# Optimization experiments

Hardware: AMD Instinct MI355X
Metric: run time of the kernel (lower is better)

## Reference

```python
import jax, jax.numpy as jnp
import numpy as np

N_NODES, N_EDGES, N_RELS, D_IN, D_OUT = 50000, 200000, 64, 32, 32


def setup_inputs() -> dict:
    key = jax.random.key(0)
    k1, k2, k3, k4, k5 = jax.random.split(key, 5)
    feat = jax.random.normal(k1, (N_NODES, D_IN), dtype=jnp.float32)
    # learned per-relation projection weights: [R, D_IN, D_OUT]
    weight = jax.random.normal(k2, (N_RELS, D_IN, D_OUT), dtype=jnp.float32) * 0.05
    src = jax.random.randint(k3, (N_EDGES,), 0, N_NODES)
    dst = jax.random.randint(k4, (N_EDGES,), 0, N_NODES)
    etypes = jax.random.randint(k5, (N_EDGES,), 0, N_RELS)
    return {"feat": feat, "weight": weight, "src": src, "dst": dst, "etypes": etypes}


def reference(feat, weight, src, dst, etypes):
    # gather source features and per-edge relation weights (HighMem variant
    # materializes W[etypes] just like torch index_select), then per-edge bmm
    n_nodes = feat.shape[0]
    msg = jnp.einsum('ei,eio->eo', feat[src], weight[etypes])  # [E, D_OUT]
    out = jax.ops.segment_sum(msg, dst, num_segments=n_nodes)  # [N, D_OUT]
    return out
```

## Files before the change

kernel.cpp:

```cpp
#include <hip/hip_runtime.h>


#define D 32
#define NRELS 64
#define BLOCK 1024
#define WPB (BLOCK / 64)
#define GRID 256
#define MAXCHUNK 1024
#define MAXTILES (NRELS + MAXCHUNK / 16)

typedef __bf16 bf16x8 __attribute__((ext_vector_type(8)));
typedef float  f32x4  __attribute__((ext_vector_type(4)));

static __device__ __forceinline__ unsigned int f2b(float x) {
    unsigned int u = __float_as_uint(x);
    return (u + 0x7fffu + ((u >> 16) & 1u)) >> 16;
}


__global__ __launch_bounds__(256) void prep_kernel(
    const float* __restrict__ feat, const float* __restrict__ weight,
    unsigned short* __restrict__ featb,
    unsigned short* __restrict__ wpack,
    int n_nodes)
{
    int idx = blockIdx.x * 256 + threadIdx.x;
    int nfeat = n_nodes * 4;
    if (idx < nfeat) {
        const float4* fp = (const float4*)(feat + (size_t)idx * 8);
        float4 a = fp[0], b = fp[1];
        uint4 o;
        o.x = f2b(a.x) | (f2b(a.y) << 16);
        o.y = f2b(a.z) | (f2b(a.w) << 16);
        o.z = f2b(b.x) | (f2b(b.y) << 16);
        o.w = f2b(b.z) | (f2b(b.w) << 16);
        ((uint4*)featb)[idx] = o;
    } else if (idx < nfeat + NRELS * 2 * 64) {
        int t = idx - nfeat;
        int r = t >> 7, half = (t >> 6) & 1, lane = t & 63;
        int quad = lane >> 4, n = lane & 15;
        const float* W = weight + (size_t)r * (D * D) + half * 16 + n;
        uint4 o;
        unsigned int v[8];
        #pragma unroll
        for (int j = 0; j < 8; ++j) v[j] = f2b(W[(quad * 8 + j) * D]);
        o.x = v[0] | (v[1] << 16);
        o.y = v[2] | (v[3] << 16);
        o.z = v[4] | (v[5] << 16);
        o.w = v[6] | (v[7] << 16);
        ((uint4*)wpack)[t] = o;
    }
}


__global__ __launch_bounds__(BLOCK, 4) void rgcn_fused_kernel(
    const unsigned short* __restrict__ featb,
    const unsigned short* __restrict__ wpack,
    const int* __restrict__ src,
    const int* __restrict__ dst,
    const int* __restrict__ etypes,
    float* __restrict__ out,
    int E, int chunk)
{
    __shared__ int cnt[NRELS];
    __shared__ int off[NRELS];
    __shared__ unsigned short list[MAXCHUNK];
    __shared__ unsigned short desc[MAXTILES];
    __shared__ int ntile_sh;

    int tid = threadIdx.x;
    int gbase = blockIdx.x * chunk;

    if (tid < NRELS) cnt[tid] = 0;
    __syncthreads();

    int my_r = -1, my_rank = 0;
    if (tid < chunk && gbase + tid < E) {
        my_r = etypes[gbase + tid];
        my_rank = atomicAdd(&cnt[my_r], 1);
    }
    __syncthreads();

    if (tid < 64) {
        int c = cnt[tid];
        int x = c;
        #pragma unroll
        for (int o = 1; o < 64; o <<= 1) {
            int y = __shfl_up(x, o, 64);
            if (tid >= o) x += y;
        }
        off[tid] = x - c;

        int nt = (c + 15) >> 4;
        int tx = nt;
        #pragma unroll
        for (int o = 1; o < 64; o <<= 1) {
            int y = __shfl_up(tx, o, 64);
            if (tid >= o) tx += y;
        }
        int tbase = tx - nt;
        for (int t = 0; t < nt; ++t)
            desc[tbase + t] = (unsigned short)((tid << 8) | t);
        if (tid == 63) ntile_sh = tx;
    }
    __syncthreads();

    if (my_r >= 0) list[off[my_r] + my_rank] = (unsigned short)tid;
    int ntiles = ntile_sh;
    __syncthreads();

    int wave = tid >> 6;
    int lane = tid & 63;
    int n    = lane & 15;
    int quad = lane >> 4;

    int per = (ntiles + WPB - 1) / WPB;
    int t0 = wave * per;
    int t1 = t0 + per; if (t1 > ntiles) t1 = ntiles;

    for (int ti = t0; ti < t1; ++ti) {
        int dsc = desc[ti];
        int r = dsc >> 8;
        int t = dsc & 255;
        int c = cnt[r];
        int mbase = t * 16;
        int mcnt = c - mbase; if (mcnt > 16) mcnt = 16;
        int lbase = off[r] + mbase;

        bf16x8 b0 = *(const bf16x8*)(wpack + ((size_t)(r * 2 + 0) * 64 + lane) * 8);
        bf16x8 b1 = *(const bf16x8*)(wpack + ((size_t)(r * 2 + 1) * 64 + lane) * 8);

        int mm = (n < mcnt) ? n : 0;
        int le = list[lbase + mm];
        int s  = src[gbase + le];
        bf16x8 a = *(const bf16x8*)(featb + (size_t)s * D + quad * 8);

        f32x4 z = {0.f, 0.f, 0.f, 0.f};
        f32x4 c0 = __builtin_amdgcn_mfma_f32_16x16x32_bf16(a, b0, z, 0, 0, 0);
        f32x4 c1 = __builtin_amdgcn_mfma_f32_16x16x32_bf16(a, b1, z, 0, 0, 0);

        #pragma unroll
        for (int v = 0; v < 4; ++v) {
            int m2 = quad * 4 + v;
            if (m2 < mcnt) {
                int le2 = list[lbase + m2];
                int d = dst[gbase + le2];
                atomicAdd(out + (size_t)d * D + n,      c0[v]);
                atomicAdd(out + (size_t)d * D + 16 + n, c1[v]);
            }
        }
    }
}


__global__ __launch_bounds__(256) void rgcn_edge_kernel(
    const float* __restrict__ feat, const float* __restrict__ weight,
    const int* __restrict__ src, const int* __restrict__ dst,
    const int* __restrict__ etypes, float* __restrict__ out, int n_edges)
{
    int gid = blockIdx.x * blockDim.x + threadIdx.x;
    int e = gid >> 5;
    int o = gid & 31;
    if (e >= n_edges) return;
    int s = src[e], d = dst[e], r = etypes[e];
    const float* W = weight + (size_t)r * (D * D);
    float fv = feat[(size_t)s * D + o];
    float acc = 0.f;
    #pragma unroll
    for (int i = 0; i < D; ++i) {
        float fi = __shfl(fv, i, 32);
        acc = fmaf(fi, W[i * D + o], acc);
    }
    atomicAdd(&out[(size_t)d * D + o], acc);
}


extern "C" void kernel_launch(void* const* d_in, const int* in_sizes, int n_in,
                              void* d_out, int out_size, void* d_ws, size_t ws_size,
                              hipStream_t stream) {
    const float* feat   = (const float*)d_in[0];
    const float* weight = (const float*)d_in[1];
    const int*   src    = (const int*)d_in[2];
    const int*   dst    = (const int*)d_in[3];
    const int*   etypes = (const int*)d_in[4];
    float*       out    = (float*)d_out;

    int N = in_sizes[0] / D;
    int R = in_sizes[1] / (D * D);
    int E = in_sizes[2];

    hipMemsetAsync(d_out, 0, (size_t)out_size * sizeof(float), stream);

    int chunk = (E + GRID - 1) / GRID;
    size_t featb_elems = (size_t)N * D;
    size_t need = (featb_elems + (size_t)NRELS * 2 * 64 * 8) * sizeof(unsigned short);

    if (R != NRELS || chunk > MAXCHUNK || ws_size < need) {
        long long total = (long long)E * 32;
        int grid = (int)((total + 255) / 256);
        rgcn_edge_kernel<<<grid, 256, 0, stream>>>(feat, weight, src, dst,
                                                   etypes, out, E);
        return;
    }

    unsigned short* featb = (unsigned short*)d_ws;
    unsigned short* wpack = featb + featb_elems;

    int prep_tasks = N * 4 + NRELS * 2 * 64;
    int prep_grid = (prep_tasks + 255) / 256;
    prep_kernel<<<prep_grid, 256, 0, stream>>>(feat, weight, featb, wpack, N);

    rgcn_fused_kernel<<<GRID, BLOCK, 0, stream>>>(featb, wpack, src, dst,
                                                  etypes, out, E, chunk);
}
```

Before: 94.25 us.

## Replace float atomic scatter with CSR-by-destination bucketing and segmented gather

Builds a per-destination histogram and a two-kernel prefix scan to get CSR offsets. Each edge gets a slot in a message buffer sorted by destination. The MFMA kernel now writes messages to those slots with plain stores instead of atomics to the output. A final gather kernel sums each node's contiguous messages. This removes the contention and cost of float atomics on the output, but adds several launches, an integer histogram with atomics, a slot-assignment atomic, and an E x 32 float staging buffer written and then read back.

```diff
diff --git a/kernel.cpp b/kernel.cpp
--- a/kernel.cpp
+++ b/kernel.cpp
@@ -20,12 +20,15 @@
 
 __global__ __launch_bounds__(256) void prep_kernel(
     const float* __restrict__ feat, const float* __restrict__ weight,
+    const int* __restrict__ dst,
     unsigned short* __restrict__ featb,
     unsigned short* __restrict__ wpack,
-    int n_nodes)
+    int* __restrict__ hist,
+    int n_nodes, int E)
 {
     int idx = blockIdx.x * 256 + threadIdx.x;
     int nfeat = n_nodes * 4;
+    int nw = NRELS * 2 * 64;
     if (idx < nfeat) {
         const float4* fp = (const float4*)(feat + (size_t)idx * 8);
         float4 a = fp[0], b = fp[1];
@@ -35,7 +38,7 @@
         o.z = f2b(b.x) | (f2b(b.y) << 16);
         o.w = f2b(b.z) | (f2b(b.w) << 16);
         ((uint4*)featb)[idx] = o;
-    } else if (idx < nfeat + NRELS * 2 * 64) {
+    } else if (idx < nfeat + nw) {
         int t = idx - nfeat;
         int r = t >> 7, half = (t >> 6) & 1, lane = t & 63;
         int quad = lane >> 4, n = lane & 15;
@@ -49,23 +52,88 @@
         o.z = v[4] | (v[5] << 16);
         o.w = v[6] | (v[7] << 16);
         ((uint4*)wpack)[t] = o;
-    }
-}
-
-
-__global__ __launch_bounds__(BLOCK, 4) void rgcn_fused_kernel(
+    } else if (idx < nfeat + nw + E) {
+        int e = idx - nfeat - nw;
+        atomicAdd(&hist[dst[e]], 1);
+    }
+}
+
+
+__global__ __launch_bounds__(256) void scan1_kernel(
+    const int* __restrict__ hist, int* __restrict__ off,
+    int* __restrict__ bsum, int N)
+{
+    __shared__ int wsum[4];
+    int t = threadIdx.x;
+    int idx = blockIdx.x * 1024 + t * 4;
+    int4 v = {0, 0, 0, 0};
+    if (idx + 3 < N) v = *(const int4*)(hist + idx);
+    else {
+        if (idx     < N) v.x = hist[idx];
+        if (idx + 1 < N) v.y = hist[idx + 1];
+        if (idx + 2 < N) v.z = hist[idx + 2];
+        if (idx + 3 < N) v.w = hist[idx + 3];
+    }
+    int s0 = v.x, s1 = s0 + v.y, s2 = s1 + v.z, s3 = s2 + v.w;
+    int x = s3;
+    #pragma unroll
+    for (int o = 1; o < 64; o <<= 1) {
+        int y = __shfl_up(x, o, 64);
+        if ((t & 63) >= o) x += y;
+    }
+    if ((t & 63) == 63) wsum[t >> 6] = x;
+    __syncthreads();
+    int w = t >> 6;
+    int wbase = 0;
+    #pragma unroll
+    for (int i = 0; i < 4; ++i) if (i < w) wbase += wsum[i];
+    int excl = wbase + x - s3;
+    if (idx     < N) off[idx]     = excl;
+    if (idx + 1 < N) off[idx + 1] = excl + s0;
+    if (idx + 2 < N) off[idx + 2] = excl + s1;
+    if (idx + 3 < N) off[idx + 3] = excl + s2;
+    if (t == 255) bsum[blockIdx.x] = wbase + x;
+}
+
+
+__global__ __launch_bounds__(256) void scan2_kernel(
+    int* __restrict__ off, const int* __restrict__ bsum,
+    int N, int E, int nblk)
+{
+    __shared__ int sbase;
+    int t = threadIdx.x;
+    if (t < 64) {
+        int v = (t < (int)blockIdx.x && t < nblk) ? bsum[t] : 0;
+        #pragma unroll
+        for (int o = 32; o > 0; o >>= 1) v += __shfl_down(v, o, 64);
+        if (t == 0) sbase = v;
+    }
+    __syncthreads();
+    int base = sbase;
+    int idx = blockIdx.x * 1024 + t * 4;
+    #pragma unroll
+    for (int k = 0; k < 4; ++k)
+        if (idx + k < N) off[idx + k] += base;
+    if (blockIdx.x == 0 && t == 0) off[N] = E;
+}
+
+
+__global__ __launch_bounds__(BLOCK, 4) void rgcn_compute_kernel(
     const unsigned short* __restrict__ featb,
     const unsigned short* __restrict__ wpack,
     const int* __restrict__ src,
     const int* __restrict__ dst,
     const int* __restrict__ etypes,
-    float* __restrict__ out,
+    const int* __restrict__ off,
+    int* __restrict__ cur,
+    float* __restrict__ msg,
     int E, int chunk)
 {
     __shared__ int cnt[NRELS];
-    __shared__ int off[NRELS];
+    __shared__ int offr[NRELS];
     __shared__ unsigned short list[MAXCHUNK];
     __shared__ unsigned short desc[MAXTILES];
+    __shared__ int slot_sh[MAXCHUNK];
     __shared__ int ntile_sh;
 
     int tid = threadIdx.x;
@@ -76,8 +144,11 @@
 
     int my_r = -1, my_rank = 0;
     if (tid < chunk && gbase + tid < E) {
-        my_r = etypes[gbase + tid];
+        int e = gbase + tid;
+        my_r = etypes[e];
         my_rank = atomicAdd(&cnt[my_r], 1);
+        int d = dst[e];
+        slot_sh[tid] = off[d] + atomicAdd(&cur[d], 1);
     }
     __syncthreads();
 
@@ -89,7 +160,7 @@
             int y = __shfl_up(x, o, 64);
             if (tid >= o) x += y;
         }
-        off[tid] = x - c;
+        offr[tid] = x - c;
 
         int nt = (c + 15) >> 4;
         int tx = nt;
@@ -105,7 +176,7 @@
     }
     __syncthreads();
 
-    if (my_r >= 0) list[off[my_r] + my_rank] = (unsigned short)tid;
+    if (my_r >= 0) list[offr[my_r] + my_rank] = (unsigned short)tid;
     int ntiles = ntile_sh;
     __syncthreads();
 
@@ -125,7 +196,7 @@
         int c = cnt[r];
         int mbase = t * 16;
         int mcnt = c - mbase; if (mcnt > 16) mcnt = 16;
-        int lbase = off[r] + mbase;
+        int lbase = offr[r] + mbase;
 
         bf16x8 b0 = *(const bf16x8*)(wpack + ((size_t)(r * 2 + 0) * 64 + lane) * 8);
         bf16x8 b1 = *(const bf16x8*)(wpack + ((size_t)(r * 2 + 1) * 64 + lane) * 8);
@@ -143,13 +214,29 @@
         for (int v = 0; v < 4; ++v) {
             int m2 = quad * 4 + v;
             if (m2 < mcnt) {
-                int le2 = list[lbase + m2];
-                int d = dst[gbase + le2];
-                atomicAdd(out + (size_t)d * D + n,      c0[v]);
-                atomicAdd(out + (size_t)d * D + 16 + n, c1[v]);
+                int s2 = slot_sh[list[lbase + m2]];
+                float* mr = msg + (size_t)s2 * D;
+                mr[n]      = c0[v];
+                mr[16 + n] = c1[v];
             }
         }
     }
+}
+
+
+__global__ __launch_bounds__(256) void gather_kernel(
+    const float* __restrict__ msg, const int* __restrict__ off,
+    float* __restrict__ out, int N)
+{
+    int d   = blockIdx.x * 8 + (threadIdx.x >> 5);
+    int col = threadIdx.x & 31;
+    if (d >= N) return;
+    int b = off[d];
+    int e = off[d + 1];
+    float acc = 0.f;
+    for (int j = b; j < e; ++j)
+        acc += msg[(size_t)j * D + col];
+    out[(size_t)d * D + col] = acc;
 }
 
 
@@ -189,13 +276,21 @@
     int R = in_sizes[1] / (D * D);
     int E = in_sizes[2];
 
-    hipMemsetAsync(d_out, 0, (size_t)out_size * sizeof(float), stream);
-
     int chunk = (E + GRID - 1) / GRID;
+    int nblk  = (N + 1023) / 1024;
+
     size_t featb_elems = (size_t)N * D;
-    size_t need = (featb_elems + (size_t)NRELS * 2 * 64 * 8) * sizeof(unsigned short);
-
-    if (R != NRELS || chunk > MAXCHUNK || ws_size < need) {
+    size_t wpack_elems = (size_t)NRELS * 2 * 64 * 8;
+    size_t hist_off = (featb_elems + wpack_elems) * sizeof(unsigned short);
+    size_t cur_off  = hist_off + (size_t)N * sizeof(int);
+    size_t off_off  = cur_off  + (size_t)N * sizeof(int);
+    size_t bsum_off = off_off  + ((size_t)N + 4) * sizeof(int);
+    size_t msg_off  = bsum_off + 64 * sizeof(int);
+    size_t need     = msg_off  + (size_t)E * D * sizeof(float);
+
+    if (R != NRELS || chunk > MAXCHUNK || nblk > 64 ||
+        (hist_off & 15) || ws_size < need) {
+        hipMemsetAsync(d_out, 0, (size_t)out_size * sizeof(float), stream);
         long long total = (long long)E * 32;
         int grid = (int)((total + 255) / 256);
         rgcn_edge_kernel<<<grid, 256, 0, stream>>>(feat, weight, src, dst,
@@ -205,11 +300,25 @@
 
     unsigned short* featb = (unsigned short*)d_ws;
     unsigned short* wpack = featb + featb_elems;
-
-    int prep_tasks = N * 4 + NRELS * 2 * 64;
+    int*   hist = (int*)((char*)d_ws + hist_off);
+    int*   cur  = (int*)((char*)d_ws + cur_off);
+    int*   offp = (int*)((char*)d_ws + off_off);
+    int*   bsum = (int*)((char*)d_ws + bsum_off);
+    float* msg  = (float*)((char*)d_ws + msg_off);
+
+    hipMemsetAsync(hist, 0, (size_t)N * 2 * sizeof(int), stream);
+
+    int prep_tasks = N * 4 + NRELS * 2 * 64 + E;
     int prep_grid = (prep_tasks + 255) / 256;
-    prep_kernel<<<prep_grid, 256, 0, stream>>>(feat, weight, featb, wpack, N);
-
-    rgcn_fused_kernel<<<GRID, BLOCK, 0, stream>>>(featb, wpack, src, dst,
-                                                  etypes, out, E, chunk);
-}
+    prep_kernel<<<prep_grid, 256, 0, stream>>>(feat, weight, dst, featb, wpack,
+                                               hist, N, E);
+
+    scan1_kernel<<<nblk, 256, 0, stream>>>(hist, offp, bsum, N);
+    scan2_kernel<<<nblk, 256, 0, stream>>>(offp, bsum, N, E, nblk);
+
+    rgcn_compute_kernel<<<GRID, BLOCK, 0, stream>>>(featb, wpack, src, dst,
+                                                    etypes, offp, cur, msg,
+                                                    E, chunk);
+
+    gather_kernel<<<(N + 7) / 8, 256, 0, stream>>>(msg, offp, out, N);
+}
```

After: 117.4 us. 24.5% more time.

## Globally bucket edges by relation before MFMA compute with spill fallback

Applied to the files above, without the earlier changes.

Replaces the per-block local sort by relation with a global bucketing pass, fused into the prep kernel, that writes edge ids into fixed-capacity per-relation lists. It adds a spill path for overflow. A new compute kernel gives each wave a fixed range of tiles for one relation, so full 16-row MFMA tiles are used instead of many partially filled per-block tiles. It also broadcasts dst indices with shuffles instead of reloading them. This costs an extra memset, global atomics on relation counters, and a workspace of 64×4096 ints, and it may leave load imbalance across waves.

```diff
diff --git a/kernel.cpp b/kernel.cpp
--- a/kernel.cpp
+++ b/kernel.cpp
@@ -3,11 +3,11 @@
 
 #define D 32
 #define NRELS 64
-#define BLOCK 1024
-#define WPB (BLOCK / 64)
-#define GRID 256
-#define MAXCHUNK 1024
-#define MAXTILES (NRELS + MAXCHUNK / 16)
+#define CAP 4096
+#define TPR (CAP / 16)
+#define SORTB 256
+#define CGRID 1024
+#define CBLOCK 256
 
 typedef __bf16 bf16x8 __attribute__((ext_vector_type(8)));
 typedef float  f32x4  __attribute__((ext_vector_type(4)));
@@ -18,25 +18,35 @@
 }
 
 
-__global__ __launch_bounds__(256) void prep_kernel(
+__global__ __launch_bounds__(256) void prep_sort_kernel(
     const float* __restrict__ feat, const float* __restrict__ weight,
+    const int* __restrict__ etypes,
     unsigned short* __restrict__ featb,
     unsigned short* __restrict__ wpack,
-    int n_nodes)
+    int* __restrict__ relcnt,
+    int* __restrict__ spillcnt,
+    int* __restrict__ slist,
+    int* __restrict__ spill,
+    int n_nodes, int E, int nbf, int chunk)
 {
-    int idx = blockIdx.x * 256 + threadIdx.x;
-    int nfeat = n_nodes * 4;
-    if (idx < nfeat) {
-        const float4* fp = (const float4*)(feat + (size_t)idx * 8);
-        float4 a = fp[0], b = fp[1];
-        uint4 o;
-        o.x = f2b(a.x) | (f2b(a.y) << 16);
-        o.y = f2b(a.z) | (f2b(a.w) << 16);
-        o.z = f2b(b.x) | (f2b(b.y) << 16);
-        o.w = f2b(b.z) | (f2b(b.w) << 16);
-        ((uint4*)featb)[idx] = o;
-    } else if (idx < nfeat + NRELS * 2 * 64) {
-        int t = idx - nfeat;
+    int b = blockIdx.x, tid = threadIdx.x;
+
+    if (b < nbf) {
+        int idx = b * 256 + tid;
+        if (idx < n_nodes * 4) {
+            const float4* fp = (const float4*)(feat + (size_t)idx * 8);
+            float4 a = fp[0], c = fp[1];
+            uint4 o;
+            o.x = f2b(a.x) | (f2b(a.y) << 16);
+            o.y = f2b(a.z) | (f2b(a.w) << 16);
+            o.z = f2b(c.x) | (f2b(c.y) << 16);
+            o.w = f2b(c.z) | (f2b(c.w) << 16);
+            ((uint4*)featb)[idx] = o;
+        }
+        return;
+    }
+    if (b < nbf + 32) {
+        int t = (b - nbf) * 256 + tid;
         int r = t >> 7, half = (t >> 6) & 1, lane = t & 63;
         int quad = lane >> 4, n = lane & 15;
         const float* W = weight + (size_t)r * (D * D) + half * 16 + n;
@@ -49,105 +59,124 @@
         o.z = v[4] | (v[5] << 16);
         o.w = v[6] | (v[7] << 16);
         ((uint4*)wpack)[t] = o;
-    }
-}
-
-
-__global__ __launch_bounds__(BLOCK, 4) void rgcn_fused_kernel(
+        return;
+    }
+
+    int sb = b - nbf - 32;
+    __shared__ int bins[NRELS];
+    __shared__ int sbase[NRELS];
+    if (tid < NRELS) bins[tid] = 0;
+    __syncthreads();
+
+    int cb = sb * chunk;
+    int ce = cb + chunk; if (ce > E) ce = E;
+    int kit = (chunk + 255) >> 8;
+
+    int myr[4], myk[4];
+    #pragma unroll
+    for (int k = 0; k < 4; ++k) {
+        myr[k] = -1;
+        int e = cb + k * 256 + tid;
+        if (k < kit && e < ce) {
+            myr[k] = etypes[e];
+            myk[k] = atomicAdd(&bins[myr[k]], 1);
+        }
+    }
+    __syncthreads();
+
+    if (tid < NRELS) {
+        int c = bins[tid];
+        sbase[tid] = c ? atomicAdd(&relcnt[tid], c) : 0;
+    }
+    __syncthreads();
+
+    #pragma unroll
+    for (int k = 0; k < 4; ++k) {
+        if (myr[k] >= 0) {
+            int e = cb + k * 256 + tid;
+            int r = myr[k];
+            int p = sbase[r] + myk[k];
+            if (p < CAP) slist[r * CAP + p] = e;
+            else { int sp = atomicAdd(spillcnt, 1); spill[sp] = e; }
+        }
+    }
+}
+
+
+__global__ __launch_bounds__(256) void rgcn_compute_kernel(
     const unsigned short* __restrict__ featb,
     const unsigned short* __restrict__ wpack,
     const int* __restrict__ src,
     const int* __restrict__ dst,
     const int* __restrict__ etypes,
-    float* __restrict__ out,
-    int E, int chunk)
+    const int* __restrict__ slist,
+    const int* __restrict__ relcnt,
+    const int* __restrict__ spill,
+    const int* __restrict__ spillcnt,
+    const float* __restrict__ feat,
+    const float* __restrict__ weight,
+    float* __restrict__ out, int E)
 {
-    __shared__ int cnt[NRELS];
-    __shared__ int off[NRELS];
-    __shared__ unsigned short list[MAXCHUNK];
-    __shared__ unsigned short desc[MAXTILES];
-    __shared__ int ntile_sh;
-
-    int tid = threadIdx.x;
-    int gbase = blockIdx.x * chunk;
-
-    if (tid < NRELS) cnt[tid] = 0;
-    __syncthreads();
-
-    int my_r = -1, my_rank = 0;
-    if (tid < chunk && gbase + tid < E) {
-        my_r = etypes[gbase + tid];
-        my_rank = atomicAdd(&cnt[my_r], 1);
-    }
-    __syncthreads();
-
-    if (tid < 64) {
-        int c = cnt[tid];
-        int x = c;
-        #pragma unroll
-        for (int o = 1; o < 64; o <<= 1) {
-            int y = __shfl_up(x, o, 64);
-            if (tid >= o) x += y;
-        }
-        off[tid] = x - c;
-
-        int nt = (c + 15) >> 4;
-        int tx = nt;
-        #pragma unroll
-        for (int o = 1; o < 64; o <<= 1) {
-            int y = __shfl_up(tx, o, 64);
-            if (tid >= o) tx += y;
-        }
-        int tbase = tx - nt;
-        for (int t = 0; t < nt; ++t)
-            desc[tbase + t] = (unsigned short)((tid << 8) | t);
-        if (tid == 63) ntile_sh = tx;
-    }
-    __syncthreads();
-
-    if (my_r >= 0) list[off[my_r] + my_rank] = (unsigned short)tid;
-    int ntiles = ntile_sh;
-    __syncthreads();
-
-    int wave = tid >> 6;
+    int tid  = threadIdx.x;
+    int wg   = blockIdx.x * (CBLOCK / 64) + (tid >> 6);
     int lane = tid & 63;
     int n    = lane & 15;
     int quad = lane >> 4;
 
-    int per = (ntiles + WPB - 1) / WPB;
-    int t0 = wave * per;
-    int t1 = t0 + per; if (t1 > ntiles) t1 = ntiles;
-
-    for (int ti = t0; ti < t1; ++ti) {
-        int dsc = desc[ti];
-        int r = dsc >> 8;
-        int t = dsc & 255;
-        int c = cnt[r];
-        int mbase = t * 16;
-        int mcnt = c - mbase; if (mcnt > 16) mcnt = 16;
-        int lbase = off[r] + mbase;
-
+    int r  = wg >> 6;
+    int t0 = (wg & 63) * (TPR / 64);
+
+    int cnt = relcnt[r]; if (cnt > CAP) cnt = CAP;
+    int ntr = (cnt + 15) >> 4;
+    int tend = t0 + (TPR / 64); if (tend > ntr) tend = ntr;
+
+    if (t0 < tend) {
         bf16x8 b0 = *(const bf16x8*)(wpack + ((size_t)(r * 2 + 0) * 64 + lane) * 8);
         bf16x8 b1 = *(const bf16x8*)(wpack + ((size_t)(r * 2 + 1) * 64 + lane) * 8);
 
-        int mm = (n < mcnt) ? n : 0;
-        int le = list[lbase + mm];
-        int s  = src[gbase + le];
-        bf16x8 a = *(const bf16x8*)(featb + (size_t)s * D + quad * 8);
-
-        f32x4 z = {0.f, 0.f, 0.f, 0.f};
-        f32x4 c0 = __builtin_amdgcn_mfma_f32_16x16x32_bf16(a, b0, z, 0, 0, 0);
-        f32x4 c1 = __builtin_amdgcn_mfma_f32_16x16x32_bf16(a, b1, z, 0, 0, 0);
-
-        #pragma unroll
-        for (int v = 0; v < 4; ++v) {
-            int m2 = quad * 4 + v;
-            if (m2 < mcnt) {
-                int le2 = list[lbase + m2];
-                int d = dst[gbase + le2];
-                atomicAdd(out + (size_t)d * D + n,      c0[v]);
-                atomicAdd(out + (size_t)d * D + 16 + n, c1[v]);
+        for (int t = t0; t < tend; ++t) {
+            int tb   = t * 16;
+            int mcnt = cnt - tb; if (mcnt > 16) mcnt = 16;
+            int base = r * CAP + tb;
+
+            int mm = (n < mcnt) ? n : (mcnt - 1);
+            int e  = slist[base + mm];
+            int s  = src[e];
+            int d  = dst[e];
+
+            bf16x8 a = *(const bf16x8*)(featb + (size_t)s * D + quad * 8);
+
+            f32x4 z = {0.f, 0.f, 0.f, 0.f};
+            f32x4 c0 = __builtin_amdgcn_mfma_f32_16x16x32_bf16(a, b0, z, 0, 0, 0);
+            f32x4 c1 = __builtin_amdgcn_mfma_f32_16x16x32_bf16(a, b1, z, 0, 0, 0);
+
+            #pragma unroll
+            for (int v = 0; v < 4; ++v) {
+                int m2 = quad * 4 + v;
+                if (m2 < mcnt) {
+                    int d2 = __shfl(d, m2, 16);
+                    atomicAdd(out + (size_t)d2 * D + n,      c0[v]);
+                    atomicAdd(out + (size_t)d2 * D + 16 + n, c1[v]);
+                }
             }
+        }
+    }
+
+    int ns = *spillcnt;
+    if (ns > 0) {
+        if (ns > E) ns = E;
+        int gsz = gridDim.x * blockDim.x;
+        for (int idx = blockIdx.x * CBLOCK + tid; idx < ns * 32; idx += gsz) {
+            int e = spill[idx >> 5];
+            int o = idx & 31;
+            int s = src[e], d = dst[e], rr = etypes[e];
+            const float* W = weight + (size_t)rr * (D * D);
+            float fv = feat[(size_t)s * D + o];
+            float acc = 0.f;
+            #pragma unroll
+            for (int i = 0; i < D; ++i)
+                acc = fmaf(__shfl(fv, i, 32), W[i * D + o], acc);
+            atomicAdd(&out[(size_t)d * D + o], acc);
         }
     }
 }
@@ -189,13 +218,18 @@
     int R = in_sizes[1] / (D * D);
     int E = in_sizes[2];
 
-    hipMemsetAsync(d_out, 0, (size_t)out_size * sizeof(float), stream);
-
-    int chunk = (E + GRID - 1) / GRID;
+    int chunk = (E + SORTB - 1) / SORTB;
+    int nbf   = (N * 4 + 255) / 256;
+
     size_t featb_elems = (size_t)N * D;
-    size_t need = (featb_elems + (size_t)NRELS * 2 * 64 * 8) * sizeof(unsigned short);
-
-    if (R != NRELS || chunk > MAXCHUNK || ws_size < need) {
+    size_t wpack_elems = (size_t)NRELS * 2 * 64 * 8;
+    size_t ctrl_off  = (featb_elems + wpack_elems) * sizeof(unsigned short);
+    size_t slist_off = ctrl_off + 80 * sizeof(int);
+    size_t spill_off = slist_off + (size_t)NRELS * CAP * sizeof(int);
+    size_t need      = spill_off + (size_t)E * sizeof(int);
+
+    if (R != NRELS || chunk > 1024 || (ctrl_off & 15) || ws_size < need) {
+        hipMemsetAsync(d_out, 0, (size_t)out_size * sizeof(float), stream);
         long long total = (long long)E * 32;
         int grid = (int)((total + 255) / 256);
         rgcn_edge_kernel<<<grid, 256, 0, stream>>>(feat, weight, src, dst,
@@ -205,11 +239,20 @@
 
     unsigned short* featb = (unsigned short*)d_ws;
     unsigned short* wpack = featb + featb_elems;
-
-    int prep_tasks = N * 4 + NRELS * 2 * 64;
-    int prep_grid = (prep_tasks + 255) / 256;
-    prep_kernel<<<prep_grid, 256, 0, stream>>>(feat, weight, featb, wpack, N);
-
-    rgcn_fused_kernel<<<GRID, BLOCK, 0, stream>>>(featb, wpack, src, dst,
-                                                  etypes, out, E, chunk);
-}
+    int* relcnt   = (int*)((char*)d_ws + ctrl_off);
+    int* spillcnt = relcnt + 64;
+    int* slist    = (int*)((char*)d_ws + slist_off);
+    int* spill    = (int*)((char*)d_ws + spill_off);
+
+    hipMemsetAsync(d_out, 0, (size_t)out_size * sizeof(float), stream);
+    hipMemsetAsync(relcnt, 0, 80 * sizeof(int), stream);
+
+    int prep_grid = nbf + 32 + SORTB;
+    prep_sort_kernel<<<prep_grid, 256, 0, stream>>>(
+        feat, weight, etypes, featb, wpack, relcnt, spillcnt, slist, spill,
+        N, E, nbf, chunk);
+
+    rgcn_compute_kernel<<<CGRID, CBLOCK, 0, stream>>>(
+        featb, wpack, src, dst, etypes, slist, relcnt, spill, spillcnt,
+        feat, weight, out, E);
+}
```

Result: slower. 101.7 us (+7.9%).
